# Performance work log

Hardware: AMD Instinct MI355X
Metric: run time of the kernel (lower is better)

## Reference

```python
import jax, jax.numpy as jnp
import numpy as np
import math

# ---- static config (must match init_kwargs / input_specs) ----
D = 1024
N_HEAD = 16
HEAD_DIM = D // N_HEAD          # 64
HALF = HEAD_DIM // 2            # rope half dim = 32
N_EXP = 8
TOP_K = 2
CAP_FACTOR = 2.0
LN_EPS = 1e-5


def _build_sin_cos(T, half_dim, dtype=jnp.float32):
    pos = jnp.arange(T, dtype=dtype)[:, None]                      # (T,1)
    inv_freq = 1.0 / (10000.0 ** (jnp.arange(0, 2 * half_dim, 2, dtype=dtype) / (2 * half_dim)))
    ang = pos * inv_freq[None, :]                                  # (T, half)
    return jnp.sin(ang), jnp.cos(ang)


def _layernorm(x, g, b):
    mu = jnp.mean(x, axis=-1, keepdims=True)
    var = jnp.mean(jnp.square(x - mu), axis=-1, keepdims=True)
    return (x - mu) * jax.lax.rsqrt(var + LN_EPS) * g + b


def _apply_rope(q, k, sin, cos):
    # q,k: (B,T,H,hd); sin,cos: (T, half)
    s = sin[None, :, None, :]
    c = cos[None, :, None, :]
    q1, q2 = q[..., :HALF], q[..., HALF:]
    k1, k2 = k[..., :HALF], k[..., HALF:]
    qr = jnp.concatenate([q1 * c - q2 * s, q1 * s + q2 * c], axis=-1)
    kr = jnp.concatenate([k1 * c - k2 * s, k1 * s + k2 * c], axis=-1)
    return qr, kr


def _attention(x, Wqkv, Wproj):
    B, T, C = x.shape
    qkv = x @ Wqkv                                                  # (B,T,3C)
    qkv = qkv.reshape(B, T, N_HEAD, 3 * HEAD_DIM)
    q, k, v = jnp.split(qkv, 3, axis=-1)                            # each (B,T,H,hd)
    sin, cos = _build_sin_cos(T, HALF)
    q, k = _apply_rope(q, k, sin, cos)
    scale = 1.0 / math.sqrt(HEAD_DIM)
    att = jnp.einsum('bqhd,bkhd->bhqk', q, k) * scale               # (B,H,T,T)
    causal = jnp.tril(jnp.ones((T, T), dtype=bool))
    att = jnp.where(causal[None, None], att, jnp.finfo(att.dtype).min)
    p = jax.nn.softmax(att, axis=-1)
    o = jnp.einsum('bhqk,bkhd->bqhd', p, v).reshape(B, T, C)
    return o @ Wproj, k, v


def _sparse_moe(flat, Wgate, W1, b1, W2, b2):
    # flat: (N, d). Eval mode: no router noise.
    N, d = flat.shape
    capacity = int(math.ceil(CAP_FACTOR * N / N_EXP))
    logits = flat @ Wgate                                           # (N,E)
    gates = jax.nn.softmax(logits, axis=-1)
    vals, inds = jax.lax.top_k(gates, TOP_K)                        # (N,k)
    flat_inds = inds.reshape(-1)                                    # (N*k,)
    flat_vals = vals.reshape(-1)
    neg = jnp.finfo(flat.dtype).min
    # per-expert assignment scores over all (token, slot) pairs
    scores = jnp.where(flat_inds[None, :] == jnp.arange(N_EXP)[:, None],
                       flat_vals[None, :], neg)                     # (E, N*k)
    top_scores, top_pos = jax.lax.top_k(scores, capacity)           # (E, cap)
    tok_idx = top_pos // TOP_K                                      # (E, cap)
    w = jnp.where(top_scores > neg, top_scores, 0.0)                # dropped slots -> 0 weight
    xe = flat[tok_idx]                                              # gather: (E, cap, d)
    h = jax.nn.gelu(jnp.einsum('ecd,edh->ech', xe, W1) + b1[:, None, :], approximate=False)
    out = jnp.einsum('ech,ehd->ecd', h, W2) + b2[:, None, :]
    out = out * w[..., None]
    final = jnp.zeros_like(flat).at[tok_idx.reshape(-1)].add(out.reshape(-1, d))
    return final


def setup_inputs() -> dict:
    key = jax.random.key(0)
    ks = jax.random.split(key, 10)
    B, T = 2, 2048
    s = 0.02
    return {
        'x': jax.random.normal(ks[0], (B, T, D), dtype=jnp.float32),
        'ln1_g': jnp.ones((D,), jnp.float32),
        'ln1_b': jnp.zeros((D,), jnp.float32),
        'ln2_g': jnp.ones((D,), jnp.float32),
        'ln2_b': jnp.zeros((D,), jnp.float32),
        'Wqkv': jax.random.normal(ks[1], (D, 3 * D), jnp.float32) * s,
        'Wproj': jax.random.normal(ks[2], (D, D), jnp.float32) * s,
        'Wgate': jax.random.normal(ks[3], (D, N_EXP), jnp.float32) * s,
        'W1': jax.random.normal(ks[4], (N_EXP, D, 4 * D), jnp.float32) * s,
        'b1': jnp.zeros((N_EXP, 4 * D), jnp.float32),
        'W2': jax.random.normal(ks[5], (N_EXP, 4 * D, D), jnp.float32) * s,
        'b2': jnp.zeros((N_EXP, D), jnp.float32),
    }


def reference(x, ln1_g, ln1_b, ln2_g, ln2_b, Wqkv, Wproj, Wgate, W1, b1, W2, b2):
    B, T, _ = x.shape
    x_norm = _layernorm(x, ln1_g, ln1_b)
    attn_out, k, v = _attention(x_norm, Wqkv, Wproj)
    x = x + attn_out
    ff_in = _layernorm(x, ln2_g, ln2_b)
    moe_out = _sparse_moe(ff_in.reshape(B * T, D), Wgate, W1, b1, W2, b2)
    x = x + moe_out.reshape(B, T, D)
    aux_loss = jnp.zeros((), x.dtype)  # eval mode
    return x, aux_loss, k, v
```

## Files before the change

kernel.cpp:

```cpp
#include <hip/hip_runtime.h>
#include <hip/hip_bf16.h>
#include <math.h>


#define TT 2048
#define NTOK 4096

typedef __attribute__((ext_vector_type(8))) short bf16x8;
typedef __attribute__((ext_vector_type(4))) float f32x4;
typedef __attribute__((ext_vector_type(16))) float f32x16;

static __device__ __forceinline__ ushort f2bf(float f) {
  union { float f; unsigned u; } v; v.f = f;
  unsigned r = v.u + 0x7FFFu + ((v.u >> 16) & 1u);
  return (ushort)(r >> 16);
}
static __device__ __forceinline__ float bf2f(ushort h) {
  union { unsigned u; float f; } v; v.u = ((unsigned)h) << 16; return v.f;
}
static __device__ __forceinline__ unsigned cvt_pk_bf16(float lo, float hi) {
  unsigned r;
  asm("v_cvt_pk_bf16_f32 %0, %1, %2" : "=v"(r) : "v"(lo), "v"(hi));
  return r;
}
static __device__ __forceinline__ void plane_swap(unsigned& a, unsigned& b) {
  asm("v_permlane32_swap_b32 %0, %1" : "+v"(a), "+v"(b));
}
static __device__ __forceinline__ float fexp2(float x) {
  float r;
  asm("v_exp_f32 %0, %1" : "=v"(r) : "v"(x));
  return r;
}

template<bool GATE>
__global__ __launch_bounds__(256)
void ln_kernel(const float* __restrict__ x, const float* __restrict__ g,
               const float* __restrict__ b, ushort* __restrict__ oh,
               ushort* __restrict__ ol, const float* __restrict__ Wg,
               int* __restrict__ te, float* __restrict__ tv, int* __restrict__ inv) {
  __shared__ float srow[1024];
  int row = blockIdx.x, tid = threadIdx.x;
  const float4* xr = (const float4*)(x + (size_t)row * 1024);
  float4 v = xr[tid];
  float s = v.x + v.y + v.z + v.w;
  #pragma unroll
  for (int off = 1; off < 64; off <<= 1) s += __shfl_xor(s, off);
  __shared__ float red1[4], red2[4];
  if ((tid & 63) == 0) red1[tid >> 6] = s;
  __syncthreads();
  float mu = (red1[0] + red1[1] + red1[2] + red1[3]) * (1.0f / 1024.0f);
  float dx = v.x - mu, dy = v.y - mu, dz = v.z - mu, dw = v.w - mu;
  float ss = dx*dx + dy*dy + dz*dz + dw*dw;
  #pragma unroll
  for (int off = 1; off < 64; off <<= 1) ss += __shfl_xor(ss, off);
  if ((tid & 63) == 0) red2[tid >> 6] = ss;
  __syncthreads();
  float var = (red2[0] + red2[1] + red2[2] + red2[3]) * (1.0f / 1024.0f);
  float inv_ = 1.0f / sqrtf(var + 1e-5f);
  float4 g4 = ((const float4*)g)[tid];
  float4 b4 = ((const float4*)b)[tid];
  float4 o4;
  o4.x = dx * inv_ * g4.x + b4.x;
  o4.y = dy * inv_ * g4.y + b4.y;
  o4.z = dz * inv_ * g4.z + b4.z;
  o4.w = dw * inv_ * g4.w + b4.w;
  size_t base = (size_t)row * 1024 + tid * 4;
  ushort h0 = f2bf(o4.x), h1 = f2bf(o4.y), h2 = f2bf(o4.z), h3 = f2bf(o4.w);
  ushort4 hh = {h0, h1, h2, h3};
  *(ushort4*)(oh + base) = hh;
  ushort4 ll = {f2bf(o4.x - bf2f(h0)), f2bf(o4.y - bf2f(h1)),
                f2bf(o4.z - bf2f(h2)), f2bf(o4.w - bf2f(h3))};
  *(ushort4*)(ol + base) = ll;
  if constexpr (GATE) {
    *(float4*)&srow[tid * 4] = o4;
    __syncthreads();
    float acc[8] = {};
    for (int i = tid; i < 1024; i += 256) {
      float xv = srow[i];
      const float4* wr = (const float4*)&Wg[i * 8];
      float4 w0 = wr[0], w1 = wr[1];
      acc[0] += xv * w0.x; acc[1] += xv * w0.y; acc[2] += xv * w0.z; acc[3] += xv * w0.w;
      acc[4] += xv * w1.x; acc[5] += xv * w1.y; acc[6] += xv * w1.z; acc[7] += xv * w1.w;
    }
    #pragma unroll
    for (int off = 1; off < 64; off <<= 1)
      #pragma unroll
      for (int qq = 0; qq < 8; ++qq) acc[qq] += __shfl_xor(acc[qq], off);
    __shared__ float red[4][8];
    if ((tid & 63) == 0)
      #pragma unroll
      for (int qq = 0; qq < 8; ++qq) red[tid >> 6][qq] = acc[qq];
    __syncthreads();
    if (tid == 0) {
      float gg[8];
      #pragma unroll
      for (int qq = 0; qq < 8; ++qq) gg[qq] = red[0][qq] + red[1][qq] + red[2][qq] + red[3][qq];
      float mx = gg[0];
      #pragma unroll
      for (int qq = 1; qq < 8; ++qq) mx = fmaxf(mx, gg[qq]);
      float sum = 0.0f;
      #pragma unroll
      for (int qq = 0; qq < 8; ++qq) { gg[qq] = expf(gg[qq] - mx); sum += gg[qq]; }
      float inv_s = 1.0f / sum;
      #pragma unroll
      for (int qq = 0; qq < 8; ++qq) gg[qq] *= inv_s;
      int e1 = 0; float v1 = gg[0];
      for (int qq = 1; qq < 8; ++qq) if (gg[qq] > v1) { v1 = gg[qq]; e1 = qq; }
      int e2 = -1; float v2 = -1.0f;
      for (int qq = 0; qq < 8; ++qq) { if (qq == e1) continue; if (gg[qq] > v2) { v2 = gg[qq]; e2 = qq; } }
      te[row * 2] = e1; te[row * 2 + 1] = e2;
      tv[row * 2] = v1; tv[row * 2 + 1] = v2;
      inv[row * 2] = -1; inv[row * 2 + 1] = -1;
    }
  }
}

__global__ void sincos_kernel(float* __restrict__ st, float* __restrict__ ct) {
  int t = blockIdx.x, j = threadIdx.x;
  double invf = pow(10000.0, -((double)(2 * j)) / 64.0);
  double ang = (double)t * invf;
  st[t * 32 + j] = (float)sin(ang);
  ct[t * 32 + j] = (float)cos(ang);
}

__global__ __launch_bounds__(256)
void vtprep_kernel(const float* __restrict__ vout, ushort* __restrict__ Vth,
                   ushort* __restrict__ Vtl) {
  __shared__ float tile[64][65];
  int t0 = blockIdx.x * 64, h = blockIdx.y, b = blockIdx.z;
  int tid = threadIdx.x;
  #pragma unroll
  for (int l = 0; l < 4; ++l) {
    int idx = l * 256 + tid;
    int r = idx >> 4, c4 = (idx & 15) * 4;
    *(float4*)&tile[r][c4] = *(const float4*)&vout[((size_t)(b * TT + t0 + r)) * 1024 + h * 64 + c4];
  }
  __syncthreads();
  int d = tid >> 2, ts = (tid & 3) * 16;
  union { bf16x8 v; ushort u[8]; } H0, H1, L0, L1;
  #pragma unroll
  for (int i = 0; i < 8; ++i) {
    float v0 = tile[ts + i][d];
    ushort hb0 = f2bf(v0);
    H0.u[i] = hb0; L0.u[i] = f2bf(v0 - bf2f(hb0));
    float v1 = tile[ts + 8 + i][d];
    ushort hb1 = f2bf(v1);
    H1.u[i] = hb1; L1.u[i] = f2bf(v1 - bf2f(hb1));
  }
  size_t basep = ((size_t)(b * 16 + h) * 64 + d) * TT + t0 + ts;
  *(bf16x8*)(Vth + basep) = H0.v;  *(bf16x8*)(Vth + basep + 8) = H1.v;
  *(bf16x8*)(Vtl + basep) = L0.v;  *(bf16x8*)(Vtl + basep + 8) = L1.v;
}

__global__ __launch_bounds__(256)
void flash11_kernel(const ushort* __restrict__ Qh, const ushort* __restrict__ Ql,
                    const ushort* __restrict__ Kh, const ushort* __restrict__ Kl,
                    const ushort* __restrict__ Vth, const ushort* __restrict__ Vtl,
                    float* __restrict__ Opart, float* __restrict__ Mpart,
                    float* __restrict__ Lpart) {
  int lin = blockIdx.x;
  int xcd = lin & 7, s = lin >> 3;
  int bh = xcd + 8 * (s / 40);
  int j = 39 - (s % 40);
  int qt, kc;
  if (j < 4)       { qt = j;                    kc = 0; }
  else if (j < 12) { qt = 4 + ((j - 4) >> 1);   kc = (j - 4) & 1; }
  else if (j < 24) { qt = 8 + (j - 12) / 3;     kc = (j - 12) % 3; }
  else             { qt = 12 + ((j - 24) >> 2); kc = (j - 24) & 3; }
  int slot = bh * 40 + j;
  int h = bh & 15, b = bh >> 4;
  int tid = threadIdx.x;
  int w = tid >> 6, lane = tid & 63;
  int q = lane & 31, LH = lane >> 5;
  size_t bT = (size_t)b * TT;
  int qglob0 = qt * 128 + w * 32;
  int qg = qglob0 + q;
  bf16x8 qH[4], qL[4];
  {
    const ushort* qph = Qh + (bT + qg) * 1024 + h * 64 + LH * 8;
    const ushort* qpl = Ql + (bT + qg) * 1024 + h * 64 + LH * 8;
    #pragma unroll
    for (int dblk = 0; dblk < 4; ++dblk) {
      qH[dblk] = *(const bf16x8*)(qph + dblk * 16);
      qL[dblk] = *(const bf16x8*)(qpl + dblk * 16);
    }
  }
  const ushort* Kbh = Kh + (size_t)bh * TT * 64;
  const ushort* Kbl = Kl + (size_t)bh * TT * 64;
  const ushort* Vbh = Vth + (size_t)bh * 64 * TT;
  const ushort* Vbl = Vtl + (size_t)bh * 64 * TT;
  f32x16 accO0 = {}, accO1 = {};
  float m = -3.402823466e38f, lsum = 0.0f;
  int kvlo = kc * 512;
  int kvhi = min(kvlo + 512, qglob0 + 32);

  auto loadK = [&](bf16x8 (&kH)[4], bf16x8 (&kL)[4], int kv0) {
    const ushort* kbh = Kbh + (size_t)(kv0 + q) * 64 + LH * 8;
    const ushort* kbl = Kbl + (size_t)(kv0 + q) * 64 + LH * 8;
    #pragma unroll
    for (int dblk = 0; dblk < 4; ++dblk) {
      kH[dblk] = *(const bf16x8*)(kbh + dblk * 16);
      kL[dblk] = *(const bf16x8*)(kbl + dblk * 16);
    }
  };

  auto tile = [&](bf16x8 (&kH)[4], bf16x8 (&kL)[4],
                  bf16x8 (&kHn)[4], bf16x8 (&kLn)[4], int kv0, bool pf) {
    bf16x8 vAH[2][2], vAL[2][2];
    #pragma unroll
    for (int dblk = 0; dblk < 2; ++dblk)
      #pragma unroll
      for (int s2 = 0; s2 < 2; ++s2) {
        size_t ad = (size_t)(dblk * 32 + q) * TT + kv0 + s2 * 16 + LH * 8;
        vAH[dblk][s2] = *(const bf16x8*)(Vbh + ad);
        vAL[dblk][s2] = *(const bf16x8*)(Vbl + ad);
      }
    f32x16 sa = {}, sb = {};
    __builtin_amdgcn_s_setprio(1);
    sa = __builtin_amdgcn_mfma_f32_32x32x16_bf16(kH[0], qH[0], sa, 0, 0, 0);
    sb = __builtin_amdgcn_mfma_f32_32x32x16_bf16(kH[2], qH[2], sb, 0, 0, 0);
    sa = __builtin_amdgcn_mfma_f32_32x32x16_bf16(kH[1], qH[1], sa, 0, 0, 0);
    sb = __builtin_amdgcn_mfma_f32_32x32x16_bf16(kH[3], qH[3], sb, 0, 0, 0);
    sa = __builtin_amdgcn_mfma_f32_32x32x16_bf16(kH[0], qL[0], sa, 0, 0, 0);
    sb = __builtin_amdgcn_mfma_f32_32x32x16_bf16(kH[2], qL[2], sb, 0, 0, 0);
    sa = __builtin_amdgcn_mfma_f32_32x32x16_bf16(kH[1], qL[1], sa, 0, 0, 0);
    sb = __builtin_amdgcn_mfma_f32_32x32x16_bf16(kH[3], qL[3], sb, 0, 0, 0);
    sa = __builtin_amdgcn_mfma_f32_32x32x16_bf16(kL[0], qH[0], sa, 0, 0, 0);
    sb = __builtin_amdgcn_mfma_f32_32x32x16_bf16(kL[2], qH[2], sb, 0, 0, 0);
    sa = __builtin_amdgcn_mfma_f32_32x32x16_bf16(kL[1], qH[1], sa, 0, 0, 0);
    sb = __builtin_amdgcn_mfma_f32_32x32x16_bf16(kL[3], qH[3], sb, 0, 0, 0);
    __builtin_amdgcn_s_setprio(0);
    if (pf) loadK(kHn, kLn, kv0 + 32);
    float p[16];
    float pmax = -3.402823466e38f;
    if (kv0 + 31 > qglob0) {
      #pragma unroll
      for (int r = 0; r < 16; ++r) {
        int kvg = kv0 + (r & 3) + 8 * (r >> 2) + 4 * LH;
        float sv = (kvg <= qg) ? (sa[r] + sb[r]) : -3.402823466e38f;
        p[r] = sv; pmax = fmaxf(pmax, sv);
      }
    } else {
      #pragma unroll
      for (int r = 0; r < 16; ++r) {
        float sv = sa[r] + sb[r];
        p[r] = sv; pmax = fmaxf(pmax, sv);
      }
    }
    pmax = fmaxf(pmax, __shfl_xor(pmax, 32));
    float mnew = fmaxf(m, pmax);
    float fsc = fexp2(m - mnew);
    float psum = 0.0f;
    #pragma unroll
    for (int r = 0; r < 16; ++r) { p[r] = fexp2(p[r] - mnew); psum += p[r]; }
    psum += __shfl_xor(psum, 32);
    lsum = lsum * fsc + psum;
    m = mnew;
    #pragma unroll
    for (int r = 0; r < 16; ++r) { accO0[r] *= fsc; accO1[r] *= fsc; }
    bf16x8 pHf[2], pLf[2];
    #pragma unroll
    for (int s2 = 0; s2 < 2; ++s2) {
      int s8 = s2 * 8;
      unsigned a  = cvt_pk_bf16(p[s8 + 0], p[s8 + 1]);
      unsigned bw = cvt_pk_bf16(p[s8 + 2], p[s8 + 3]);
      unsigned c  = cvt_pk_bf16(p[s8 + 4], p[s8 + 5]);
      unsigned d  = cvt_pk_bf16(p[s8 + 6], p[s8 + 7]);
      float l0 = p[s8 + 0] - __uint_as_float(a << 16);
      float l1 = p[s8 + 1] - __uint_as_float(a & 0xFFFF0000u);
      float l2 = p[s8 + 2] - __uint_as_float(bw << 16);
      float l3 = p[s8 + 3] - __uint_as_float(bw & 0xFFFF0000u);
      float l4 = p[s8 + 4] - __uint_as_float(c << 16);
      float l5 = p[s8 + 5] - __uint_as_float(c & 0xFFFF0000u);
      float l6 = p[s8 + 6] - __uint_as_float(d << 16);
      float l7 = p[s8 + 7] - __uint_as_float(d & 0xFFFF0000u);
      unsigned al = cvt_pk_bf16(l0, l1);
      unsigned bl = cvt_pk_bf16(l2, l3);
      unsigned cl = cvt_pk_bf16(l4, l5);
      unsigned dl = cvt_pk_bf16(l6, l7);
      plane_swap(a, c); plane_swap(bw, d);
      plane_swap(al, cl); plane_swap(bl, dl);
      union { unsigned w[4]; bf16x8 v; } PH, PL;
      PH.w[0] = a;  PH.w[1] = bw; PH.w[2] = c;  PH.w[3] = d;
      PL.w[0] = al; PL.w[1] = bl; PL.w[2] = cl; PL.w[3] = dl;
      pHf[s2] = PH.v; pLf[s2] = PL.v;
    }
    __builtin_amdgcn_s_setprio(1);
    #pragma unroll
    for (int s2 = 0; s2 < 2; ++s2) {
      accO0 = __builtin_amdgcn_mfma_f32_32x32x16_bf16(vAH[0][s2], pHf[s2], accO0, 0, 0, 0);
      accO1 = __builtin_amdgcn_mfma_f32_32x32x16_bf16(vAH[1][s2], pHf[s2], accO1, 0, 0, 0);
      accO0 = __builtin_amdgcn_mfma_f32_32x32x16_bf16(vAH[0][s2], pLf[s2], accO0, 0, 0, 0);
      accO1 = __builtin_amdgcn_mfma_f32_32x32x16_bf16(vAH[1][s2], pLf[s2], accO1, 0, 0, 0);
      accO0 = __builtin_amdgcn_mfma_f32_32x32x16_bf16(vAL[0][s2], pHf[s2], accO0, 0, 0, 0);
      accO1 = __builtin_amdgcn_mfma_f32_32x32x16_bf16(vAL[1][s2], pHf[s2], accO1, 0, 0, 0);
    }
    __builtin_amdgcn_s_setprio(0);
  };

  bf16x8 kA[4], kB[4], kC[4], kD[4];
  loadK(kA, kB, kvlo);
  for (int kv0 = kvlo; kv0 < kvhi; kv0 += 64) {
    tile(kA, kB, kC, kD, kv0, kv0 + 32 < kvhi);
    if (kv0 + 32 < kvhi)
      tile(kC, kD, kA, kB, kv0 + 32, kv0 + 64 < kvhi);
  }

  if (LH == 0) {
    Mpart[slot * 128 + w * 32 + q] = m;
    Lpart[slot * 128 + w * 32 + q] = lsum;
  }
  float* Ob = Opart + (size_t)slot * 8192 + (w * 32 + q) * 64;
  #pragma unroll
  for (int g2 = 0; g2 < 4; ++g2) {
    float4 v0 = {accO0[g2 * 4 + 0], accO0[g2 * 4 + 1], accO0[g2 * 4 + 2], accO0[g2 * 4 + 3]};
    *(float4*)(Ob + 8 * g2 + 4 * LH) = v0;
    float4 v1 = {accO1[g2 * 4 + 0], accO1[g2 * 4 + 1], accO1[g2 * 4 + 2], accO1[g2 * 4 + 3]};
    *(float4*)(Ob + 32 + 8 * g2 + 4 * LH) = v1;
  }
}

__global__ __launch_bounds__(256)
void fmerge2_kernel(const float* __restrict__ Opart, const float* __restrict__ Mpart,
                    const float* __restrict__ Lpart, ushort* __restrict__ oh,
                    ushort* __restrict__ ol) {
  int qt = blockIdx.x, bh = blockIdx.y;
  int h = bh & 15, b = bh >> 4;
  int g = qt >> 2;
  int nc = g + 1;
  int off = 2 * g * (g + 1) + (qt & 3) * (g + 1);
  int slot0 = bh * 40 + off;
  int tid = threadIdx.x;
  int q = tid & 127, dh = tid >> 7;
  float mg = -3.402823466e38f;
  for (int c = 0; c < nc; ++c) mg = fmaxf(mg, Mpart[(slot0 + c) * 128 + q]);
  float lg = 0.0f;
  float4 acc[8] = {};
  for (int c = 0; c < nc; ++c) {
    float sc = fexp2(Mpart[(slot0 + c) * 128 + q] - mg);
    lg += sc * Lpart[(slot0 + c) * 128 + q];
    const float4* op = (const float4*)(Opart + (size_t)(slot0 + c) * 8192 + q * 64 + dh * 32);
    #pragma unroll
    for (int i = 0; i < 8; ++i) {
      float4 v = op[i];
      acc[i].x += sc * v.x; acc[i].y += sc * v.y;
      acc[i].z += sc * v.z; acc[i].w += sc * v.w;
    }
  }
  float inv = 1.0f / lg;
  size_t obase = ((size_t)(b * TT + qt * 128 + q)) * 1024 + h * 64 + dh * 32;
  #pragma unroll
  for (int i = 0; i < 8; ++i) {
    float4 v = {acc[i].x * inv, acc[i].y * inv, acc[i].z * inv, acc[i].w * inv};
    ushort h0 = f2bf(v.x), h1 = f2bf(v.y), h2 = f2bf(v.z), h3 = f2bf(v.w);
    ushort4 hh = {h0, h1, h2, h3};
    *(ushort4*)(oh + obase + i * 4) = hh;
    ushort4 ll = {f2bf(v.x - bf2f(h0)), f2bf(v.y - bf2f(h1)),
                  f2bf(v.z - bf2f(h2)), f2bf(v.w - bf2f(h3))};
    *(ushort4*)(ol + obase + i * 4) = ll;
  }
}

template<bool LO>
__global__ void tconv_kernel(const float* __restrict__ in, ushort* __restrict__ oh,
                             ushort* __restrict__ ol, int K, int N) {
  __shared__ float t[32][33];
  int z = blockIdx.z;
  const float* ip = in + (size_t)z * K * N;
  ushort* ohp = oh + (size_t)z * K * N;
  ushort* olp = LO ? (ol + (size_t)z * K * N) : nullptr;
  int n0 = blockIdx.x * 32, k0 = blockIdx.y * 32;
  int tx = threadIdx.x, ty = threadIdx.y;
  #pragma unroll
  for (int i = 0; i < 4; ++i)
    t[ty + 8 * i][tx] = ip[(size_t)(k0 + ty + 8 * i) * N + n0 + tx];
  __syncthreads();
  #pragma unroll
  for (int i = 0; i < 4; ++i) {
    float v = t[tx][ty + 8 * i];
    size_t off = (size_t)(n0 + ty + 8 * i) * K + k0 + tx;
    ushort hb = f2bf(v);
    ohp[off] = hb;
    if (LO) olp[off] = f2bf(v - bf2f(hb));
  }
}

__global__ __launch_bounds__(256)
void tconv4_kernel(const float* __restrict__ in, ushort* __restrict__ out,
                   int K, int N) {
  __shared__ float t[64][68];
  int z = blockIdx.z;
  const float* ip = in + (size_t)z * K * N;
  ushort* op = out + (size_t)z * K * N;
  int n0 = blockIdx.x * 64, k0 = blockIdx.y * 64;
  int tid = threadIdx.x;
  int r = tid >> 4, c4 = (tid & 15) * 4;
  #pragma unroll
  for (int i = 0; i < 4; ++i)
    *(float4*)&t[r + 16 * i][c4] = *(const float4*)&ip[(size_t)(k0 + r + 16 * i) * N + n0 + c4];
  __syncthreads();
  int n = tid >> 2, kb = (tid & 3) * 16;
  union { ushort u[16]; ushort4 v[4]; } o;
  #pragma unroll
  for (int i = 0; i < 16; ++i) o.u[i] = f2bf(t[kb + i][n]);
  size_t ob = (size_t)(n0 + n) * K + k0 + kb;
  #pragma unroll
  for (int i = 0; i < 4; ++i) *(ushort4*)&op[ob + 4 * i] = o.v[i];
}

#define LOAD_STEP(tt) do {                                                     \
    int kk = (tt) << 6;                                                        \
    _Pragma("unroll")                                                          \
    for (int q = 0; q < 4; ++q) {                                              \
      int rr = r0 + 32 * q;                                                    \
      int clog = cph ^ (rr & 7);                                               \
      raH[q] = *(const bf16x8*)(AhB + (size_t)garow[q] * K + kk + clog * 8);   \
      rbH[q] = *(const bf16x8*)(BhB + (size_t)(bn + rr) * K + kk + clog * 8);  \
      if constexpr (SPLIT3) {                                                  \
        raL[q] = *(const bf16x8*)(AlB + (size_t)garow[q] * K + kk + clog * 8); \
        rbL[q] = *(const bf16x8*)(BlB + (size_t)(bn + rr) * K + kk + clog * 8);\
      }                                                                        \
    }                                                                          \
  } while (0)

template<int EPI, bool GATHER, bool SPLIT3>
__global__ __launch_bounds__(256, 2)
void mgemm(const ushort* __restrict__ Ah, const ushort* __restrict__ Al,
           const ushort* __restrict__ Bh, const ushort* __restrict__ Bl,
           void* __restrict__ Cv, const float* __restrict__ extra,
           const int* __restrict__ gatAll, int N, int K,
           long aEStride, long bEStride, long cEStride, int biasEStride,
           const float* __restrict__ st, const float* __restrict__ ct,
           float* __restrict__ kout, float* __restrict__ vout,
           ushort* __restrict__ Kh, ushort* __restrict__ Kl,
           ushort* __restrict__ Qh, ushort* __restrict__ Ql) {
  __shared__ ushort As[(SPLIT3 ? 2 : 1) * 128 * 64];
  __shared__ ushort Bs[(SPLIT3 ? 2 : 1) * 128 * 64];
  ushort* AsH = As;  ushort* AsL = SPLIT3 ? (As + 128 * 64) : As;
  ushort* BsH = Bs;  ushort* BsL = SPLIT3 ? (Bs + 128 * 64) : Bs;
  int z = blockIdx.z;
  const ushort* AhB = Ah + (size_t)z * aEStride;
  const ushort* AlB = SPLIT3 ? (Al + (size_t)z * aEStride) : nullptr;
  const ushort* BhB = Bh + (size_t)z * bEStride;
  const ushort* BlB = SPLIT3 ? (Bl + (size_t)z * bEStride) : nullptr;
  const int* gat = GATHER ? (gatAll + z * 1024) : nullptr;
  int bx = blockIdx.x, by = blockIdx.y;
  {
    int nwg = gridDim.x * gridDim.y;
    if ((nwg & 7) == 0) {
      int lid = bx + by * gridDim.x;
      int cpx = nwg >> 3;
      int wgid = (lid & 7) * cpx + (lid >> 3);
      bx = wgid % gridDim.x;
      by = wgid / gridDim.x;
    }
  }
  int bm = by * 128, bn = bx * 128;
  int tid = threadIdx.x;
  int r0 = tid >> 3, cph = tid & 7;
  int garow[4];
  #pragma unroll
  for (int q = 0; q < 4; ++q) {
    int rr = r0 + 32 * q;
    garow[q] = GATHER ? gat[bm + rr] : (bm + rr);
  }
  int kSteps = K >> 6;
  int wid = tid >> 6, lane = tid & 63;
  int wm = wid >> 1, wn = wid & 1;
  int lr = lane & 15, lk = lane >> 4;
  f32x4 acc[4][4] = {};
  bf16x8 raH[4], rbH[4], raL[4], rbL[4];
  LOAD_STEP(0);
  for (int t = 0; t < kSteps; ++t) {
    __syncthreads();
    #pragma unroll
    for (int q = 0; q < 4; ++q) {
      int rr = r0 + 32 * q;
      *(bf16x8*)&AsH[rr * 64 + cph * 8] = raH[q];
      *(bf16x8*)&BsH[rr * 64 + cph * 8] = rbH[q];
      if constexpr (SPLIT3) {
        *(bf16x8*)&AsL[rr * 64 + cph * 8] = raL[q];
        *(bf16x8*)&BsL[rr * 64 + cph * 8] = rbL[q];
      }
    }
    __syncthreads();
    if (t + 1 < kSteps) LOAD_STEP(t + 1);
    #pragma unroll
    for (int kh = 0; kh < 2; ++kh) {
      bf16x8 afH[4], bfH[4], afL[4], bfL[4];
      #pragma unroll
      for (int mf = 0; mf < 4; ++mf) {
        int row = wm * 64 + mf * 16 + lr;
        int ch = (kh * 4 + lk) ^ (row & 7);
        afH[mf] = *(const bf16x8*)&AsH[row * 64 + ch * 8];
        if constexpr (SPLIT3) afL[mf] = *(const bf16x8*)&AsL[row * 64 + ch * 8];
      }
      #pragma unroll
      for (int nf = 0; nf < 4; ++nf) {
        int row = wn * 64 + nf * 16 + lr;
        int ch = (kh * 4 + lk) ^ (row & 7);
        bfH[nf] = *(const bf16x8*)&BsH[row * 64 + ch * 8];
        if constexpr (SPLIT3) bfL[nf] = *(const bf16x8*)&BsL[row * 64 + ch * 8];
      }
      #pragma unroll
      for (int mf = 0; mf < 4; ++mf)
        #pragma unroll
        for (int nf = 0; nf < 4; ++nf)
          acc[mf][nf] = __builtin_amdgcn_mfma_f32_16x16x32_bf16(afH[mf], bfH[nf], acc[mf][nf], 0, 0, 0);
      if constexpr (SPLIT3) {
        #pragma unroll
        for (int mf = 0; mf < 4; ++mf)
          #pragma unroll
          for (int nf = 0; nf < 4; ++nf)
            acc[mf][nf] = __builtin_amdgcn_mfma_f32_16x16x32_bf16(afH[mf], bfL[nf], acc[mf][nf], 0, 0, 0);
        #pragma unroll
        for (int mf = 0; mf < 4; ++mf)
          #pragma unroll
          for (int nf = 0; nf < 4; ++nf)
            acc[mf][nf] = __builtin_amdgcn_mfma_f32_16x16x32_bf16(afL[mf], bfH[nf], acc[mf][nf], 0, 0, 0);
      }
    }
  }
  int crow = bm + wm * 64, ccol = bn + wn * 64;
  if constexpr (EPI <= 1) {
    float* C = (float*)Cv;
    #pragma unroll
    for (int mf = 0; mf < 4; ++mf)
      #pragma unroll
      for (int nf = 0; nf < 4; ++nf)
        #pragma unroll
        for (int r = 0; r < 4; ++r) {
          int row = crow + mf * 16 + lk * 4 + r;
          int col = ccol + nf * 16 + lr;
          float v = acc[mf][nf][r];
          if constexpr (EPI == 1) v += extra[(size_t)row * N + col];
          C[(size_t)row * N + col] = v;
        }
  } else if constexpr (EPI == 4) {
    const float qs = 0.125f * 1.44269504088896340736f;
    int seg = (ccol >> 6) % 3;
    int hh = ccol / 192;
    if (seg == 2) {
      #pragma unroll
      for (int mf = 0; mf < 4; ++mf)
        #pragma unroll
        for (int r = 0; r < 4; ++r) {
          int row = crow + mf * 16 + lk * 4 + r;
          size_t ob = (size_t)row * 1024 + hh * 64;
          #pragma unroll
          for (int nf = 0; nf < 4; ++nf)
            vout[ob + nf * 16 + lr] = acc[mf][nf][r];
        }
    } else if (seg == 0) {
      #pragma unroll
      for (int mf = 0; mf < 4; ++mf)
        #pragma unroll
        for (int r = 0; r < 4; ++r) {
          int row = crow + mf * 16 + lk * 4 + r;
          int t = row & (TT - 1);
          size_t qb = (size_t)row * 1024 + hh * 64;
          #pragma unroll
          for (int nf0 = 0; nf0 < 2; ++nf0) {
            int j = nf0 * 16 + lr;
            float s = st[t * 32 + j], c = ct[t * 32 + j];
            float q1 = acc[mf][nf0][r], q2 = acc[mf][nf0 + 2][r];
            float a1 = (q1 * c - q2 * s) * qs;
            float a2 = (q1 * s + q2 * c) * qs;
            ushort u1 = f2bf(a1);
            Qh[qb + j] = u1; Ql[qb + j] = f2bf(a1 - bf2f(u1));
            ushort u2 = f2bf(a2);
            Qh[qb + 32 + j] = u2; Ql[qb + 32 + j] = f2bf(a2 - bf2f(u2));
          }
        }
    } else {
      #pragma unroll
      for (int mf = 0; mf < 4; ++mf)
        #pragma unroll
        for (int r = 0; r < 4; ++r) {
          int row = crow + mf * 16 + lk * 4 + r;
          int t = row & (TT - 1);
          int bb = row >> 11;
          size_t kb = ((size_t)(bb * 16 + hh) * TT + t) * 64;
          size_t ob = (size_t)row * 1024 + hh * 64;
          #pragma unroll
          for (int nf0 = 0; nf0 < 2; ++nf0) {
            int j = nf0 * 16 + lr;
            float s = st[t * 32 + j], c = ct[t * 32 + j];
            float k1 = acc[mf][nf0][r], k2 = acc[mf][nf0 + 2][r];
            float kr1 = k1 * c - k2 * s;
            float kr2 = k1 * s + k2 * c;
            kout[ob + j] = kr1; kout[ob + 32 + j] = kr2;
            ushort u1 = f2bf(kr1);
            Kh[kb + j] = u1; Kl[kb + j] = f2bf(kr1 - bf2f(u1));
            ushort u2 = f2bf(kr2);
            Kh[kb + 32 + j] = u2; Kl[kb + 32 + j] = f2bf(kr2 - bf2f(u2));
          }
        }
    }
  } else {
    const float* bias = extra + (size_t)z * biasEStride;
    ushort* C = (ushort*)Cv + (size_t)z * cEStride;
    #pragma unroll
    for (int mf = 0; mf < 4; ++mf)
      #pragma unroll
      for (int nf = 0; nf < 4; ++nf)
        #pragma unroll
        for (int r = 0; r < 4; ++r) {
          int row = crow + mf * 16 + lk * 4 + r;
          int col = ccol + nf * 16 + lr;
          float v = acc[mf][nf][r] + bias[col];
          if constexpr (EPI == 2)
            v = 0.5f * v * (1.0f + erff(v * 0.70710678118654752f));
          C[(size_t)row * N + col] = f2bf(v);
        }
  }
}

__global__ __launch_bounds__(1024)
void route_sort_kernel(const int* __restrict__ te, const float* __restrict__ tv,
                       int* __restrict__ etok, float* __restrict__ ew,
                       int* __restrict__ inv) {
  __shared__ unsigned long long sk[4096];
  __shared__ int wcnt[16];
  __shared__ int base;
  int e = blockIdx.x, tid = threadIdx.x;
  int lane = tid & 63, wv = tid >> 6;
  if (tid == 0) base = 0;
  __syncthreads();
  for (int c = 0; c < 8; ++c) {
    int s = c * 1024 + tid;
    bool sel = (te[s] == e);
    unsigned long long ball = __ballot(sel);
    int pre = __popcll(ball & ((1ull << lane) - 1ull));
    if (lane == 0) wcnt[wv] = __popcll(ball);
    __syncthreads();
    int woff = 0, tot = 0;
    #pragma unroll
    for (int i = 0; i < 16; ++i) {
      int cc = wcnt[i];
      if (i < wv) woff += cc;
      tot += cc;
    }
    if (sel) {
      unsigned vb = __float_as_uint(tv[s]);
      sk[base + woff + pre] =
          ((unsigned long long)vb << 32) | (unsigned)(0xFFFFFFFFu - (unsigned)s);
    }
    __syncthreads();
    if (tid == 0) base += tot;
    __syncthreads();
  }
  int n = base;
  if (n > 1024) {
    int P = (n <= 2048) ? 2048 : 4096;
    for (int i = n + tid; i < P; i += 1024) sk[i] = 0ull;
    __syncthreads();
    for (int k = 2; k <= P; k <<= 1)
      for (int j = k >> 1; j > 0; j >>= 1) {
        for (int t = tid; t < (P >> 1); t += 1024) {
          int i = ((t & ~(j - 1)) << 1) | (t & (j - 1));
          int p = i | j;
          unsigned long long a = sk[i], bq = sk[p];
          bool desc = ((i & k) == 0);
          if (desc ? (a < bq) : (a > bq)) { sk[i] = bq; sk[p] = a; }
        }
        __syncthreads();
      }
  }
  int cap = n < 1024 ? n : 1024;
  if (tid < cap) {
    unsigned long long key = sk[tid];
    unsigned slot = 0xFFFFFFFFu - (unsigned)(key & 0xFFFFFFFFull);
    etok[e * 1024 + tid] = (int)(slot >> 1);
    ew[e * 1024 + tid] = __uint_as_float((unsigned)(key >> 32));
    inv[slot] = e * 1024 + tid;
  } else {
    etok[e * 1024 + tid] = 0;
    ew[e * 1024 + tid] = 0.0f;
  }
}

__global__ __launch_bounds__(256)
void combine_kernel(const float* __restrict__ xres, const ushort* __restrict__ eo,
                    const int* __restrict__ inv, const float* __restrict__ ew,
                    float* __restrict__ outx, float* __restrict__ aux) {
  int token = blockIdx.x;
  int d = threadIdx.x * 4;
  float4 acc = *(const float4*)&xres[(size_t)token * 1024 + d];
  #pragma unroll
  for (int j = 0; j < 2; ++j) {
    int p = inv[token * 2 + j];
    if (p >= 0) {
      float w = ew[p];
      const ushort* ep = eo + (size_t)p * 1024 + d;
      acc.x += w * bf2f(ep[0]); acc.y += w * bf2f(ep[1]);
      acc.z += w * bf2f(ep[2]); acc.w += w * bf2f(ep[3]);
    }
  }
  *(float4*)&outx[(size_t)token * 1024 + d] = acc;
  if (token == 0 && threadIdx.x == 0) aux[0] = 0.0f;
}

extern "C" void kernel_launch(void* const* d_in, const int* in_sizes, int n_in,
                              void* d_out, int out_size, void* d_ws, size_t ws_size,
                              hipStream_t stream) {
  const float* x     = (const float*)d_in[0];
  const float* ln1g  = (const float*)d_in[1];
  const float* ln1b  = (const float*)d_in[2];
  const float* ln2g  = (const float*)d_in[3];
  const float* ln2b  = (const float*)d_in[4];
  const float* Wqkv  = (const float*)d_in[5];
  const float* Wproj = (const float*)d_in[6];
  const float* Wg    = (const float*)d_in[7];
  const float* W1    = (const float*)d_in[8];
  const float* b1    = (const float*)d_in[9];
  const float* W2    = (const float*)d_in[10];
  const float* b2    = (const float*)d_in[11];

  float* out_x   = (float*)d_out;
  float* out_aux = out_x + 4194304;
  float* out_k   = out_aux + 1;
  float* out_v   = out_k + 4194304;

  float* ws   = (float*)d_ws;
  float* A    = ws;
  ushort* KhQ = (ushort*)(ws + 4194304);
  ushort* KlQ = KhQ + 4194304;
  ushort* Qh_ = (ushort*)(ws + 16777216);
  ushort* Ql_ = (ushort*)(ws + 18874368);
  float* st   = ws + 20971520;
  float* ct   = ws + 21037056;
  int*   te   = (int*)(ws + 21102592);
  float* tv   = ws + 21110784;
  int*   etok = (int*)(ws + 21118976);
  float* ew   = ws + 21127168;
  int*   inv  = (int*)(ws + 21135360);
  ushort* bfAh = (ushort*)(ws + 21143552);
  ushort* bfAl = (ushort*)(ws + 23240704);
  ushort* BqH  = (ushort*)(ws + 25337856);
  ushort* BqL  = (ushort*)(ws + 26910720);
  ushort* BpH  = (ushort*)(ws + 28483584);
  ushort* BpL  = (ushort*)(ws + 29007872);
  ushort* W1t  = (ushort*)(ws + 29532160);
  ushort* W2t  = (ushort*)(ws + 46309376);
  ushort* eo   = (ushort*)(ws + 63086592);
  ushort* hbuf = (ushort*)(ws + 4194304);
  ushort* Vth_ = eo;
  ushort* Vtl_ = eo + 4194304;
  float* Opart = ws + 29532160;
  float* Mpart = ws + 40017920;
  float* Lpart = ws + 40181760;
  float* vbuf  = ws + 8388608;

  tconv_kernel<true ><<<dim3(96, 32, 1),  dim3(32, 8), 0, stream>>>(Wqkv,  BqH, BqL, 1024, 3072);
  tconv_kernel<true ><<<dim3(32, 32, 1),  dim3(32, 8), 0, stream>>>(Wproj, BpH, BpL, 1024, 1024);
  sincos_kernel<<<TT, 32, 0, stream>>>(st, ct);

  ln_kernel<false><<<NTOK, 256, 0, stream>>>(x, ln1g, ln1b, bfAh, bfAl,
                                             nullptr, nullptr, nullptr, nullptr);
  mgemm<4, false, true><<<dim3(24, 32, 1), 256, 0, stream>>>(
      bfAh, bfAl, BqH, BqL, nullptr, nullptr, nullptr, 3072, 1024, 0, 0, 0, 0,
      st, ct, out_k, out_v, KhQ, KlQ, Qh_, Ql_);
  vtprep_kernel<<<dim3(32, 16, 2), 256, 0, stream>>>(out_v, Vth_, Vtl_);
  (void)vbuf;
  flash11_kernel<<<1280, 256, 0, stream>>>(Qh_, Ql_, KhQ, KlQ, Vth_, Vtl_,
                                           Opart, Mpart, Lpart);
  fmerge2_kernel<<<dim3(16, 32), 256, 0, stream>>>(Opart, Mpart, Lpart, bfAh, bfAl);
  mgemm<1, false, true><<<dim3(8, 32, 1), 256, 0, stream>>>(
      bfAh, bfAl, BpH, BpL, A, x, nullptr, 1024, 1024, 0, 0, 0, 0,
      nullptr, nullptr, nullptr, nullptr, nullptr, nullptr, nullptr, nullptr);
  tconv4_kernel<<<dim3(64, 16, 8), 256, 0, stream>>>(W1, W1t, 1024, 4096);
  tconv4_kernel<<<dim3(16, 64, 8), 256, 0, stream>>>(W2, W2t, 4096, 1024);
  ln_kernel<true><<<NTOK, 256, 0, stream>>>(A, ln2g, ln2b, bfAh, bfAl, Wg, te, tv, inv);
  route_sort_kernel<<<8, 1024, 0, stream>>>(te, tv, etok, ew, inv);
  mgemm<2, true, false><<<dim3(32, 8, 8), 256, 0, stream>>>(
      bfAh, nullptr, W1t, nullptr, hbuf, b1, etok, 4096, 1024,
      0, 4096L * 1024, 1024L * 4096, 4096,
      nullptr, nullptr, nullptr, nullptr, nullptr, nullptr, nullptr, nullptr);
  mgemm<3, false, false><<<dim3(8, 8, 8), 256, 0, stream>>>(
      hbuf, nullptr, W2t, nullptr, eo, b2, nullptr, 1024, 4096,
      1024L * 4096, 1024L * 4096, 1024L * 1024, 1024,
      nullptr, nullptr, nullptr, nullptr, nullptr, nullptr, nullptr, nullptr);
  combine_kernel<<<NTOK, 256, 0, stream>>>(A, eo, inv, ew, out_x, out_aux);
}
```

Baseline: 652.2 us.

## Use direct global-to-LDS double-buffered loads in MoE expert GEMMs

Adds a separate GEMM kernel for the two MoE expert matmuls. It uses global_load_lds to copy tiles straight into double-buffered shared memory, so the next k-step is prefetched while the current one runs on the MFMA units. This removes the register staging round trip and one barrier per step. The split-precision mgemm is trimmed to serve only the attention GEMMs. LDS use doubles per block for the new kernel, which may reduce occupancy, and the swizzled destination layout has to line up with the lane ordering of the direct LDS loads.

```diff
diff --git a/kernel.cpp b/kernel.cpp
--- a/kernel.cpp
+++ b/kernel.cpp
@@ -30,6 +30,11 @@
   float r;
   asm("v_exp_f32 %0, %1" : "=v"(r) : "v"(x));
   return r;
+}
+static __device__ __forceinline__ void gload16(const void* g, void* l) {
+  __builtin_amdgcn_global_load_lds(
+      (const __attribute__((address_space(1))) void*)g,
+      (__attribute__((address_space(3))) void*)l, 16, 0, 0);
 }
 
 template<bool GATE>
@@ -416,34 +421,28 @@
       int clog = cph ^ (rr & 7);                                               \
       raH[q] = *(const bf16x8*)(AhB + (size_t)garow[q] * K + kk + clog * 8);   \
       rbH[q] = *(const bf16x8*)(BhB + (size_t)(bn + rr) * K + kk + clog * 8);  \
-      if constexpr (SPLIT3) {                                                  \
-        raL[q] = *(const bf16x8*)(AlB + (size_t)garow[q] * K + kk + clog * 8); \
-        rbL[q] = *(const bf16x8*)(BlB + (size_t)(bn + rr) * K + kk + clog * 8);\
-      }                                                                        \
+      raL[q] = *(const bf16x8*)(AlB + (size_t)garow[q] * K + kk + clog * 8);   \
+      rbL[q] = *(const bf16x8*)(BlB + (size_t)(bn + rr) * K + kk + clog * 8);  \
     }                                                                          \
   } while (0)
 
-template<int EPI, bool GATHER, bool SPLIT3>
+template<int EPI>
 __global__ __launch_bounds__(256, 2)
 void mgemm(const ushort* __restrict__ Ah, const ushort* __restrict__ Al,
            const ushort* __restrict__ Bh, const ushort* __restrict__ Bl,
-           void* __restrict__ Cv, const float* __restrict__ extra,
-           const int* __restrict__ gatAll, int N, int K,
-           long aEStride, long bEStride, long cEStride, int biasEStride,
+           void* __restrict__ Cv, const float* __restrict__ extra, int N, int K,
            const float* __restrict__ st, const float* __restrict__ ct,
            float* __restrict__ kout, float* __restrict__ vout,
            ushort* __restrict__ Kh, ushort* __restrict__ Kl,
            ushort* __restrict__ Qh, ushort* __restrict__ Ql) {
-  __shared__ ushort As[(SPLIT3 ? 2 : 1) * 128 * 64];
-  __shared__ ushort Bs[(SPLIT3 ? 2 : 1) * 128 * 64];
-  ushort* AsH = As;  ushort* AsL = SPLIT3 ? (As + 128 * 64) : As;
-  ushort* BsH = Bs;  ushort* BsL = SPLIT3 ? (Bs + 128 * 64) : Bs;
-  int z = blockIdx.z;
-  const ushort* AhB = Ah + (size_t)z * aEStride;
-  const ushort* AlB = SPLIT3 ? (Al + (size_t)z * aEStride) : nullptr;
-  const ushort* BhB = Bh + (size_t)z * bEStride;
-  const ushort* BlB = SPLIT3 ? (Bl + (size_t)z * bEStride) : nullptr;
-  const int* gat = GATHER ? (gatAll + z * 1024) : nullptr;
+  __shared__ ushort As[2 * 128 * 64];
+  __shared__ ushort Bs[2 * 128 * 64];
+  ushort* AsH = As;  ushort* AsL = As + 128 * 64;
+  ushort* BsH = Bs;  ushort* BsL = Bs + 128 * 64;
+  const ushort* AhB = Ah;
+  const ushort* AlB = Al;
+  const ushort* BhB = Bh;
+  const ushort* BlB = Bl;
   int bx = blockIdx.x, by = blockIdx.y;
   {
     int nwg = gridDim.x * gridDim.y;
@@ -460,10 +459,7 @@
   int r0 = tid >> 3, cph = tid & 7;
   int garow[4];
   #pragma unroll
-  for (int q = 0; q < 4; ++q) {
-    int rr = r0 + 32 * q;
-    garow[q] = GATHER ? gat[bm + rr] : (bm + rr);
-  }
+  for (int q = 0; q < 4; ++q) garow[q] = bm + r0 + 32 * q;
   int kSteps = K >> 6;
   int wid = tid >> 6, lane = tid & 63;
   int wm = wid >> 1, wn = wid & 1;
@@ -478,10 +474,8 @@
       int rr = r0 + 32 * q;
       *(bf16x8*)&AsH[rr * 64 + cph * 8] = raH[q];
       *(bf16x8*)&BsH[rr * 64 + cph * 8] = rbH[q];
-      if constexpr (SPLIT3) {
-        *(bf16x8*)&AsL[rr * 64 + cph * 8] = raL[q];
-        *(bf16x8*)&BsL[rr * 64 + cph * 8] = rbL[q];
-      }
+      *(bf16x8*)&AsL[rr * 64 + cph * 8] = raL[q];
+      *(bf16x8*)&BsL[rr * 64 + cph * 8] = rbL[q];
     }
     __syncthreads();
     if (t + 1 < kSteps) LOAD_STEP(t + 1);
@@ -493,36 +487,34 @@
         int row = wm * 64 + mf * 16 + lr;
         int ch = (kh * 4 + lk) ^ (row & 7);
         afH[mf] = *(const bf16x8*)&AsH[row * 64 + ch * 8];
-        if constexpr (SPLIT3) afL[mf] = *(const bf16x8*)&AsL[row * 64 + ch * 8];
+        afL[mf] = *(const bf16x8*)&AsL[row * 64 + ch * 8];
       }
       #pragma unroll
       for (int nf = 0; nf < 4; ++nf) {
         int row = wn * 64 + nf * 16 + lr;
         int ch = (kh * 4 + lk) ^ (row & 7);
         bfH[nf] = *(const bf16x8*)&BsH[row * 64 + ch * 8];
-        if constexpr (SPLIT3) bfL[nf] = *(const bf16x8*)&BsL[row * 64 + ch * 8];
+        bfL[nf] = *(const bf16x8*)&BsL[row * 64 + ch * 8];
       }
       #pragma unroll
       for (int mf = 0; mf < 4; ++mf)
         #pragma unroll
         for (int nf = 0; nf < 4; ++nf)
           acc[mf][nf] = __builtin_amdgcn_mfma_f32_16x16x32_bf16(afH[mf], bfH[nf], acc[mf][nf], 0, 0, 0);
-      if constexpr (SPLIT3) {
+      #pragma unroll
+      for (int mf = 0; mf < 4; ++mf)
         #pragma unroll
-        for (int mf = 0; mf < 4; ++mf)
-          #pragma unroll
-          for (int nf = 0; nf < 4; ++nf)
-            acc[mf][nf] = __builtin_amdgcn_mfma_f32_16x16x32_bf16(afH[mf], bfL[nf], acc[mf][nf], 0, 0, 0);
+        for (int nf = 0; nf < 4; ++nf)
+          acc[mf][nf] = __builtin_amdgcn_mfma_f32_16x16x32_bf16(afH[mf], bfL[nf], acc[mf][nf], 0, 0, 0);
+      #pragma unroll
+      for (int mf = 0; mf < 4; ++mf)
         #pragma unroll
-        for (int mf = 0; mf < 4; ++mf)
-          #pragma unroll
-          for (int nf = 0; nf < 4; ++nf)
-            acc[mf][nf] = __builtin_amdgcn_mfma_f32_16x16x32_bf16(afL[mf], bfH[nf], acc[mf][nf], 0, 0, 0);
-      }
+        for (int nf = 0; nf < 4; ++nf)
+          acc[mf][nf] = __builtin_amdgcn_mfma_f32_16x16x32_bf16(afL[mf], bfH[nf], acc[mf][nf], 0, 0, 0);
     }
   }
   int crow = bm + wm * 64, ccol = bn + wn * 64;
-  if constexpr (EPI <= 1) {
+  if constexpr (EPI == 1) {
     float* C = (float*)Cv;
     #pragma unroll
     for (int mf = 0; mf < 4; ++mf)
@@ -532,11 +524,9 @@
         for (int r = 0; r < 4; ++r) {
           int row = crow + mf * 16 + lk * 4 + r;
           int col = ccol + nf * 16 + lr;
-          float v = acc[mf][nf][r];
-          if constexpr (EPI == 1) v += extra[(size_t)row * N + col];
-          C[(size_t)row * N + col] = v;
+          C[(size_t)row * N + col] = acc[mf][nf][r] + extra[(size_t)row * N + col];
         }
-  } else if constexpr (EPI == 4) {
+  } else {
     const float qs = 0.125f * 1.44269504088896340736f;
     int seg = (ccol >> 6) % 3;
     int hh = ccol / 192;
@@ -597,23 +587,107 @@
           }
         }
     }
-  } else {
-    const float* bias = extra + (size_t)z * biasEStride;
-    ushort* C = (ushort*)Cv + (size_t)z * cEStride;
-    #pragma unroll
-    for (int mf = 0; mf < 4; ++mf)
-      #pragma unroll
-      for (int nf = 0; nf < 4; ++nf)
+  }
+}
+
+#define STAGE_ND(buf, tt) do {                                                 \
+    int kk = (tt) << 6;                                                        \
+    _Pragma("unroll")                                                          \
+    for (int i = 0; i < 4; ++i) {                                              \
+      int row = w32 + i * 8 + lrow;                                            \
+      int sc = cph2 ^ (row & 7);                                               \
+      gload16(AB + (size_t)garow[i] * K + kk + sc * 8,                         \
+              &As[buf][(w32 + i * 8) * 64]);                                   \
+      gload16(BB + (size_t)(bn + row) * K + kk + sc * 8,                       \
+              &Bs[buf][(w32 + i * 8) * 64]);                                   \
+    }                                                                          \
+  } while (0)
+
+template<int EPI, bool GATHER>
+__global__ __launch_bounds__(256, 2)
+void mgemm_nd(const ushort* __restrict__ Ah, const ushort* __restrict__ Bh,
+              ushort* __restrict__ Cv, const float* __restrict__ extra,
+              const int* __restrict__ gatAll, int N, int K,
+              long aEStride, long bEStride, long cEStride, int biasEStride) {
+  __shared__ ushort As[2][128 * 64];
+  __shared__ ushort Bs[2][128 * 64];
+  int z = blockIdx.z;
+  const ushort* AB = Ah + (size_t)z * aEStride;
+  const ushort* BB = Bh + (size_t)z * bEStride;
+  const int* gat = GATHER ? (gatAll + z * 1024) : nullptr;
+  int bx = blockIdx.x, by = blockIdx.y;
+  {
+    int nwg = gridDim.x * gridDim.y;
+    if ((nwg & 7) == 0) {
+      int lid = bx + by * gridDim.x;
+      int cpx = nwg >> 3;
+      int wgid = (lid & 7) * cpx + (lid >> 3);
+      bx = wgid % gridDim.x;
+      by = wgid / gridDim.x;
+    }
+  }
+  int bm = by * 128, bn = bx * 128;
+  int tid = threadIdx.x;
+  int wid = tid >> 6, lane = tid & 63;
+  int w32 = wid * 32;
+  int lrow = lane >> 3, cph2 = lane & 7;
+  int garow[4];
+  #pragma unroll
+  for (int i = 0; i < 4; ++i) {
+    int row = w32 + i * 8 + lrow;
+    garow[i] = GATHER ? gat[bm + row] : (bm + row);
+  }
+  int kSteps = K >> 6;
+  int wm = wid >> 1, wn = wid & 1;
+  int lr = lane & 15, lk = lane >> 4;
+  f32x4 acc[4][4] = {};
+
+  STAGE_ND(0, 0);
+  asm volatile("s_waitcnt vmcnt(0)" ::: "memory");
+  __builtin_amdgcn_s_barrier();
+  for (int t = 0; t < kSteps; ++t) {
+    int cur = t & 1;
+    if (t + 1 < kSteps) STAGE_ND(cur ^ 1, t + 1);
+    #pragma unroll
+    for (int kh = 0; kh < 2; ++kh) {
+      bf16x8 af[4], bfr[4];
+      #pragma unroll
+      for (int mf = 0; mf < 4; ++mf) {
+        int row = wm * 64 + mf * 16 + lr;
+        int ch = (kh * 4 + lk) ^ (row & 7);
+        af[mf] = *(const bf16x8*)&As[cur][row * 64 + ch * 8];
+      }
+      #pragma unroll
+      for (int nf = 0; nf < 4; ++nf) {
+        int row = wn * 64 + nf * 16 + lr;
+        int ch = (kh * 4 + lk) ^ (row & 7);
+        bfr[nf] = *(const bf16x8*)&Bs[cur][row * 64 + ch * 8];
+      }
+      #pragma unroll
+      for (int mf = 0; mf < 4; ++mf)
         #pragma unroll
-        for (int r = 0; r < 4; ++r) {
-          int row = crow + mf * 16 + lk * 4 + r;
-          int col = ccol + nf * 16 + lr;
-          float v = acc[mf][nf][r] + bias[col];
-          if constexpr (EPI == 2)
-            v = 0.5f * v * (1.0f + erff(v * 0.70710678118654752f));
-          C[(size_t)row * N + col] = f2bf(v);
-        }
-  }
+        for (int nf = 0; nf < 4; ++nf)
+          acc[mf][nf] = __builtin_amdgcn_mfma_f32_16x16x32_bf16(af[mf], bfr[nf], acc[mf][nf], 0, 0, 0);
+    }
+    asm volatile("s_waitcnt vmcnt(0)" ::: "memory");
+    __builtin_amdgcn_s_barrier();
+  }
+  int crow = bm + wm * 64, ccol = bn + wn * 64;
+  const float* bias = extra + (size_t)z * biasEStride;
+  ushort* C = Cv + (size_t)z * cEStride;
+  #pragma unroll
+  for (int mf = 0; mf < 4; ++mf)
+    #pragma unroll
+    for (int nf = 0; nf < 4; ++nf)
+      #pragma unroll
+      for (int r = 0; r < 4; ++r) {
+        int row = crow + mf * 16 + lk * 4 + r;
+        int col = ccol + nf * 16 + lr;
+        float v = acc[mf][nf][r] + bias[col];
+        if constexpr (EPI == 2)
+          v = 0.5f * v * (1.0f + erff(v * 0.70710678118654752f));
+        C[(size_t)row * N + col] = f2bf(v);
+      }
 }
 
 __global__ __launch_bounds__(1024)
@@ -750,7 +824,6 @@
   float* Opart = ws + 29532160;
   float* Mpart = ws + 40017920;
   float* Lpart = ws + 40181760;
-  float* vbuf  = ws + 8388608;
 
   tconv_kernel<true ><<<dim3(96, 32, 1),  dim3(32, 8), 0, stream>>>(Wqkv,  BqH, BqL, 1024, 3072);
   tconv_kernel<true ><<<dim3(32, 32, 1),  dim3(32, 8), 0, stream>>>(Wproj, BpH, BpL, 1024, 1024);
@@ -758,28 +831,25 @@
 
   ln_kernel<false><<<NTOK, 256, 0, stream>>>(x, ln1g, ln1b, bfAh, bfAl,
                                              nullptr, nullptr, nullptr, nullptr);
-  mgemm<4, false, true><<<dim3(24, 32, 1), 256, 0, stream>>>(
-      bfAh, bfAl, BqH, BqL, nullptr, nullptr, nullptr, 3072, 1024, 0, 0, 0, 0,
+  mgemm<4><<<dim3(24, 32, 1), 256, 0, stream>>>(
+      bfAh, bfAl, BqH, BqL, nullptr, nullptr, 3072, 1024,
       st, ct, out_k, out_v, KhQ, KlQ, Qh_, Ql_);
   vtprep_kernel<<<dim3(32, 16, 2), 256, 0, stream>>>(out_v, Vth_, Vtl_);
-  (void)vbuf;
   flash11_kernel<<<1280, 256, 0, stream>>>(Qh_, Ql_, KhQ, KlQ, Vth_, Vtl_,
                                            Opart, Mpart, Lpart);
   fmerge2_kernel<<<dim3(16, 32), 256, 0, stream>>>(Opart, Mpart, Lpart, bfAh, bfAl);
-  mgemm<1, false, true><<<dim3(8, 32, 1), 256, 0, stream>>>(
-      bfAh, bfAl, BpH, BpL, A, x, nullptr, 1024, 1024, 0, 0, 0, 0,
+  mgemm<1><<<dim3(8, 32, 1), 256, 0, stream>>>(
+      bfAh, bfAl, BpH, BpL, A, x, 1024, 1024,
       nullptr, nullptr, nullptr, nullptr, nullptr, nullptr, nullptr, nullptr);
   tconv4_kernel<<<dim3(64, 16, 8), 256, 0, stream>>>(W1, W1t, 1024, 4096);
   tconv4_kernel<<<dim3(16, 64, 8), 256, 0, stream>>>(W2, W2t, 4096, 1024);
   ln_kernel<true><<<NTOK, 256, 0, stream>>>(A, ln2g, ln2b, bfAh, bfAl, Wg, te, tv, inv);
   route_sort_kernel<<<8, 1024, 0, stream>>>(te, tv, etok, ew, inv);
-  mgemm<2, true, false><<<dim3(32, 8, 8), 256, 0, stream>>>(
-      bfAh, nullptr, W1t, nullptr, hbuf, b1, etok, 4096, 1024,
-      0, 4096L * 1024, 1024L * 4096, 4096,
-      nullptr, nullptr, nullptr, nullptr, nullptr, nullptr, nullptr, nullptr);
-  mgemm<3, false, false><<<dim3(8, 8, 8), 256, 0, stream>>>(
-      hbuf, nullptr, W2t, nullptr, eo, b2, nullptr, 1024, 4096,
-      1024L * 4096, 1024L * 4096, 1024L * 1024, 1024,
-      nullptr, nullptr, nullptr, nullptr, nullptr, nullptr, nullptr, nullptr);
+  mgemm_nd<2, true><<<dim3(32, 8, 8), 256, 0, stream>>>(
+      bfAh, W1t, hbuf, b1, etok, 4096, 1024,
+      0, 4096L * 1024, 1024L * 4096, 4096);
+  mgemm_nd<3, false><<<dim3(8, 8, 8), 256, 0, stream>>>(
+      hbuf, W2t, eo, b2, nullptr, 1024, 4096,
+      1024L * 4096, 1024L * 4096, 1024L * 1024, 1024);
   combine_kernel<<<NTOK, 256, 0, stream>>>(A, eo, inv, ew, out_x, out_aux);
 }
```

New measurement: 695.2 us. +6.6%, slower.
